# Kernel optimization log

Hardware: AMD Instinct MI355X
Metric: run time of the kernel (lower is better)

## Reference

```python
import jax, jax.numpy as jnp
import numpy as np

PI2 = 6.283185307


def setup_inputs() -> dict:
    key = jax.random.key(0)
    k1, k2, k3, k4 = jax.random.split(key, 4)
    T, n_mix, n_dim = 262144, 64, 16
    data = jax.random.normal(k1, (T, n_dim), dtype=jnp.float32)
    # mixture weights: positive, roughly summing to 1
    wghts = jax.random.uniform(k2, (n_mix, 1), dtype=jnp.float32, minval=0.5, maxval=1.5) / n_mix
    means = jax.random.normal(k3, (n_mix, n_dim), dtype=jnp.float32)
    # diagonal covariances: strictly positive
    dcovs = jax.random.uniform(k4, (n_mix, n_dim), dtype=jnp.float32, minval=0.5, maxval=1.5)
    return {"data": data, "wghts": wghts, "means": means, "dcovs": dcovs}


def reference(data, wghts, means, dcovs):
    # data: (T, D); wghts: (M, 1); means: (M, D); dcovs: (M, D)
    n_dim = data.shape[1]
    c = 1.0 / np.sqrt(PI2 ** n_dim)  # Gaussian normalizer (2*pi)^{-D/2}
    c_dets = 1.0 / jnp.sqrt(jnp.prod(dcovs, axis=1))  # (M,) |Sigma|^{-1/2}
    dprecs = 1.0 / dcovs  # (M, D) diagonal precisions
    diff = data[:, None, :] - means[None, :, :]  # (T, M, D)
    mhbs_dist = jnp.einsum('tmd,md->tm', diff * diff, dprecs)  # (T, M)
    probs = (wghts[:, 0] * c * c_dets)[None, :] * jnp.exp(-0.5 * mhbs_dist)  # (T, M)
    likes = jnp.sum(probs, axis=1)  # (T,)
    log_likes = jnp.mean(jnp.log(likes))
    posteriors = probs / likes[:, None]  # (T, M)
    e_means = posteriors @ means  # (T, D) weighted mean of component means
    return (log_likes, e_means)
```

## Files before the change

kernel.cpp:

```cpp
#include <hip/hip_runtime.h>

#define T_TOTAL 262144
#define NBLOCKS 1024
#define NMIX 64
#define NDIM 16

typedef short bf16x8 __attribute__((ext_vector_type(8)));
typedef unsigned short u16x8 __attribute__((ext_vector_type(8)));
typedef unsigned short u16x4 __attribute__((ext_vector_type(4)));
typedef float f32x4 __attribute__((ext_vector_type(4)));

__device__ __forceinline__ unsigned short f2bf(float f) {
    union { float f; unsigned u; } v; v.f = f;
    unsigned r = v.u + 0x7fff + ((v.u >> 16) & 1);
    return (unsigned short)(r >> 16);
}
__device__ __forceinline__ float bf2f(unsigned short s) {
    union { unsigned u; float f; } v; v.u = ((unsigned)s) << 16;
    return v.f;
}

#define L_WH   0
#define L_WL   5120
#define L_MUT  10240
#define L_A2   12544
#define L_RED  12800
#define L_P    12864

__global__ __launch_bounds__(256, 4) void gmm_main(const float* __restrict__ data,
                                                   const float* __restrict__ wghts,
                                                   const float* __restrict__ means,
                                                   const float* __restrict__ dcovs,
                                                   float* __restrict__ out,
                                                   float* __restrict__ part) {
    __shared__ __align__(16) char lds[22080];
    const int tid  = threadIdx.x;
    const int w    = tid >> 6;
    const int lane = tid & 63;
    const int gi   = lane & 15;
    const int gq   = lane >> 4;
    const size_t tblk = (size_t)blockIdx.x * 256;

    {
        const int m  = tid >> 2;
        const int ql = tid & 3;
        const float LOG2E = 1.4426950408889634f;
        const float LOG2_2PI = 2.6514961294723187f;
        const float4 d4 = *(const float4*)(dcovs + m * 16 + ql * 4);
        const float4 m4 = *(const float4*)(means + m * 16 + ql * 4);
        const float wm = wghts[m];
        float dc[4] = {d4.x, d4.y, d4.z, d4.w};
        float mu[4] = {m4.x, m4.y, m4.z, m4.w};
        u16x4 ghv, glv, hhv, hlv;
        float sumlog = 0.0f, qsum = 0.0f;
        unsigned short* mut = (unsigned short*)(lds + L_MUT);
#pragma unroll
        for (int j = 0; j < 4; ++j) {
            float pr = __builtin_amdgcn_rcpf(dc[j]);
            float g = -0.5f * LOG2E * pr;
            float h = LOG2E * pr * mu[j];
            unsigned short gH = f2bf(g), hH = f2bf(h);
            ghv[j] = gH;  glv[j] = f2bf(g - bf2f(gH));
            hhv[j] = hH;  hlv[j] = f2bf(h - bf2f(hH));
            mut[(ql * 4 + j) * 72 + m] = f2bf(mu[j]);
            sumlog += __builtin_amdgcn_logf(dc[j]);
            qsum   += pr * mu[j] * mu[j];
        }
        char* wrh = lds + L_WH + m * 80;
        char* wrl = lds + L_WL + m * 80;
        *(u16x4*)(wrh + ql * 8)      = ghv;
        *(u16x4*)(wrh + 32 + ql * 8) = hhv;
        *(u16x4*)(wrl + ql * 8)      = glv;
        *(u16x4*)(wrl + 32 + ql * 8) = hlv;
        sumlog += __shfl_xor(sumlog, 1); sumlog += __shfl_xor(sumlog, 2);
        qsum   += __shfl_xor(qsum, 1);   qsum   += __shfl_xor(qsum, 2);
        if (ql == 0) {
            float log2C = __builtin_amdgcn_logf(wm) - 8.0f * LOG2_2PI - 0.5f * sumlog;
            ((float*)(lds + L_A2))[m] = log2C - 0.5f * LOG2E * qsum;
        }
    }
    __syncthreads();

    bf16x8 bh[4], bl[4];
    float a2v[4];
#pragma unroll
    for (int c = 0; c < 4; ++c) {
        bh[c] = *(const bf16x8*)(lds + L_WH + (c * 16 + gi) * 80 + gq * 16);
        bl[c] = *(const bf16x8*)(lds + L_WL + (c * 16 + gi) * 80 + gq * 16);
        a2v[c] = ((const float*)(lds + L_A2))[c * 16 + gi];
    }
    bf16x8 mf0 = *(const bf16x8*)(lds + L_MUT + gi * 144 + gq * 16);
    bf16x8 mf1 = *(const bf16x8*)(lds + L_MUT + gi * 144 + 64 + gq * 16);

    char* pbase = lds + L_P + w * 2304;
    float ll_acc = 0.0f;

    const float* xbase = data + (tblk + (size_t)w * 64 + gi) * 16 + (gq & 1) * 8;
    float4 xa = *(const float4*)(xbase);
    float4 xb = *(const float4*)(xbase + 4);
    const bool sq = (gq < 2);

#pragma unroll
    for (int rt = 0; rt < 4; ++rt) {
        float4 na, nb;
        if (rt < 3) {
            na = *(const float4*)(xbase + (rt + 1) * 256);
            nb = *(const float4*)(xbase + (rt + 1) * 256 + 4);
        }

        float xv[8] = {xa.x, xa.y, xa.z, xa.w, xb.x, xb.y, xb.z, xb.w};
        u16x8 ahv, alv;
#pragma unroll
        for (int j = 0; j < 8; ++j) {
            float q = sq ? xv[j] * xv[j] : xv[j];
            unsigned short qh = f2bf(q);
            ahv[j] = qh;
            alv[j] = f2bf(q - bf2f(qh));
        }
        bf16x8 ah = *(bf16x8*)&ahv;
        bf16x8 al = *(bf16x8*)&alv;

        f32x4 pacc[4];
#pragma unroll
        for (int c = 0; c < 4; ++c) {
            f32x4 a = {0.0f, 0.0f, 0.0f, 0.0f};
            a = __builtin_amdgcn_mfma_f32_16x16x32_bf16(al, bh[c], a, 0, 0, 0);
            a = __builtin_amdgcn_mfma_f32_16x16x32_bf16(ah, bl[c], a, 0, 0, 0);
            a = __builtin_amdgcn_mfma_f32_16x16x32_bf16(ah, bh[c], a, 0, 0, 0);
            pacc[c] = a;
        }

        float p[4][4], prow[4], inv[4];
#pragma unroll
        for (int reg = 0; reg < 4; ++reg) {
#pragma unroll
            for (int c = 0; c < 4; ++c)
                p[c][reg] = __builtin_amdgcn_exp2f(pacc[c][reg] + a2v[c]);
            prow[reg] = (p[0][reg] + p[1][reg]) + (p[2][reg] + p[3][reg]);
        }
#pragma unroll
        for (int reg = 0; reg < 4; ++reg) {
            float v = prow[reg];
            v += __shfl_xor(v, 1);  v += __shfl_xor(v, 2);
            v += __shfl_xor(v, 4);  v += __shfl_xor(v, 8);
            v = fmaxf(v, 1e-35f);
            ll_acc += __builtin_amdgcn_logf(v);
            inv[reg] = __builtin_amdgcn_rcpf(v);
        }

#pragma unroll
        for (int c = 0; c < 4; ++c)
#pragma unroll
            for (int reg = 0; reg < 4; ++reg)
                *(unsigned short*)(pbase + (gq * 4 + reg) * 144 + (c * 16 + gi) * 2) =
                    f2bf(p[c][reg]);

        bf16x8 ap0 = *(const bf16x8*)(pbase + gi * 144 + gq * 16);
        bf16x8 ap1 = *(const bf16x8*)(pbase + gi * 144 + 64 + gq * 16);
        f32x4 e = {0.0f, 0.0f, 0.0f, 0.0f};
        e = __builtin_amdgcn_mfma_f32_16x16x32_bf16(ap0, mf0, e, 0, 0, 0);
        e = __builtin_amdgcn_mfma_f32_16x16x32_bf16(ap1, mf1, e, 0, 0, 0);

        size_t trow = tblk + (size_t)w * 64 + rt * 16 + gq * 4;
#pragma unroll
        for (int reg = 0; reg < 4; ++reg)
            out[1 + (trow + reg) * 16 + gi] = e[reg] * inv[reg];

        if (rt < 3) { xa = na; xb = nb; }
    }

    ll_acc += __shfl_xor(ll_acc, 16);
    ll_acc += __shfl_xor(ll_acc, 32);
    if (lane == 0) ((float*)(lds + L_RED))[w] = ll_acc;
    __syncthreads();
    if (tid == 0) {
        float* r = (float*)(lds + L_RED);
        part[blockIdx.x] = (r[0] + r[1]) + (r[2] + r[3]);
    }
}

__global__ void gmm_fin(const float* __restrict__ part, float* __restrict__ out) {
    __shared__ double red[4];
    const int tid = threadIdx.x;
    double s = 0.0;
#pragma unroll
    for (int k = 0; k < 4; ++k) s += (double)part[tid + k * 256];
#pragma unroll
    for (int off = 32; off > 0; off >>= 1) s += __shfl_down(s, off, 64);
    const int wv = tid >> 6, lane = tid & 63;
    if (lane == 0) red[wv] = s;
    __syncthreads();
    if (tid == 0) {
        const double LN2 = 0.6931471805599453;
        double tot = (red[0] + red[1]) + (red[2] + red[3]);
        out[0] = (float)(tot * LN2 / (double)T_TOTAL);
    }
}

extern "C" void kernel_launch(void* const* d_in, const int* in_sizes, int n_in,
                              void* d_out, int out_size, void* d_ws, size_t ws_size,
                              hipStream_t stream) {
    const float* data  = (const float*)d_in[0];
    const float* wghts = (const float*)d_in[1];
    const float* means = (const float*)d_in[2];
    const float* dcovs = (const float*)d_in[3];
    float* out  = (float*)d_out;
    float* part = (float*)d_ws;

    gmm_main<<<NBLOCKS, 256, 0, stream>>>(data, wghts, means, dcovs, out, part);
    gmm_fin<<<1, 256, 0, stream>>>(part, out);
}
```

Measured before the change: 82.79 us.

## Fuse final reduction via last-block atomic and micro-optimize bf16 packing

Drops the separate finalize kernel: each block publishes its partial log-likelihood to a global array, and the last block to arrive (found with an atomic counter) does the double-precision reduction and resets the counter. Float-to-bf16 splitting now uses the packed v_cvt_pk_bf16_f32 instruction, the per-component bias is folded into the MFMA accumulator initialisation, and the row-sum shuffles become DPP adds. This removes one kernel launch and some VALU work. The cost is a global counter that carries state between calls, plus reliance on inline asm and DPP control encodings.

Result: slower. 142.5 us (+72.1%).

```diff
diff --git a/kernel.cpp b/kernel.cpp
--- a/kernel.cpp
+++ b/kernel.cpp
@@ -9,6 +9,7 @@
 typedef unsigned short u16x8 __attribute__((ext_vector_type(8)));
 typedef unsigned short u16x4 __attribute__((ext_vector_type(4)));
 typedef float f32x4 __attribute__((ext_vector_type(4)));
+typedef unsigned u32x4 __attribute__((ext_vector_type(4)));
 
 __device__ __forceinline__ unsigned short f2bf(float f) {
     union { float f; unsigned u; } v; v.f = f;
@@ -19,21 +20,42 @@
     union { unsigned u; float f; } v; v.u = ((unsigned)s) << 16;
     return v.f;
 }
+__device__ __forceinline__ unsigned cvt_pk(float lo, float hi) {
+    unsigned r;
+    asm("v_cvt_pk_bf16_f32 %0, %1, %2" : "=v"(r) : "v"(lo), "v"(hi));
+    return r;
+}
+__device__ __forceinline__ float f_lo(unsigned w) {
+    union { unsigned u; float f; } v; v.u = w << 16; return v.f;
+}
+__device__ __forceinline__ float f_hi(unsigned w) {
+    union { unsigned u; float f; } v; v.u = w & 0xFFFF0000u; return v.f;
+}
+template<int CTRL>
+__device__ __forceinline__ float dpp_add(float v) {
+    union { float f; int i; } s, t;
+    s.f = v;
+    t.i = __builtin_amdgcn_update_dpp(0, s.i, CTRL, 0xf, 0xf, true);
+    return v + t.f;
+}
+
+__device__ float    g_part[NBLOCKS];
+__device__ unsigned g_count;
 
 #define L_WH   0
 #define L_WL   5120
 #define L_MUT  10240
 #define L_A2   12544
 #define L_RED  12800
-#define L_P    12864
+#define L_DRED 12864
+#define L_P    12896
 
 __global__ __launch_bounds__(256, 4) void gmm_main(const float* __restrict__ data,
                                                    const float* __restrict__ wghts,
                                                    const float* __restrict__ means,
                                                    const float* __restrict__ dcovs,
-                                                   float* __restrict__ out,
-                                                   float* __restrict__ part) {
-    __shared__ __align__(16) char lds[22080];
+                                                   float* __restrict__ out) {
+    __shared__ __align__(16) char lds[22112];
     const int tid  = threadIdx.x;
     const int w    = tid >> 6;
     const int lane = tid & 63;
@@ -109,21 +131,24 @@
         }
 
         float xv[8] = {xa.x, xa.y, xa.z, xa.w, xb.x, xb.y, xb.z, xb.w};
-        u16x8 ahv, alv;
-#pragma unroll
-        for (int j = 0; j < 8; ++j) {
-            float q = sq ? xv[j] * xv[j] : xv[j];
-            unsigned short qh = f2bf(q);
-            ahv[j] = qh;
-            alv[j] = f2bf(q - bf2f(qh));
-        }
-        bf16x8 ah = *(bf16x8*)&ahv;
-        bf16x8 al = *(bf16x8*)&alv;
+        u32x4 ahw, alw;
+#pragma unroll
+        for (int jp = 0; jp < 4; ++jp) {
+            float q0 = sq ? xv[2 * jp] * xv[2 * jp]         : xv[2 * jp];
+            float q1 = sq ? xv[2 * jp + 1] * xv[2 * jp + 1] : xv[2 * jp + 1];
+            unsigned h = cvt_pk(q0, q1);
+            ahw[jp] = h;
+            alw[jp] = cvt_pk(q0 - f_lo(h), q1 - f_hi(h));
+        }
+        union { u32x4 wv; bf16x8 hv; } pa, pl;
+        pa.wv = ahw;  pl.wv = alw;
+        bf16x8 ah = pa.hv;
+        bf16x8 al = pl.hv;
 
         f32x4 pacc[4];
 #pragma unroll
         for (int c = 0; c < 4; ++c) {
-            f32x4 a = {0.0f, 0.0f, 0.0f, 0.0f};
+            f32x4 a = {a2v[c], a2v[c], a2v[c], a2v[c]};
             a = __builtin_amdgcn_mfma_f32_16x16x32_bf16(al, bh[c], a, 0, 0, 0);
             a = __builtin_amdgcn_mfma_f32_16x16x32_bf16(ah, bl[c], a, 0, 0, 0);
             a = __builtin_amdgcn_mfma_f32_16x16x32_bf16(ah, bh[c], a, 0, 0, 0);
@@ -135,25 +160,32 @@
         for (int reg = 0; reg < 4; ++reg) {
 #pragma unroll
             for (int c = 0; c < 4; ++c)
-                p[c][reg] = __builtin_amdgcn_exp2f(pacc[c][reg] + a2v[c]);
+                p[c][reg] = __builtin_amdgcn_exp2f(pacc[c][reg]);
             prow[reg] = (p[0][reg] + p[1][reg]) + (p[2][reg] + p[3][reg]);
         }
 #pragma unroll
         for (int reg = 0; reg < 4; ++reg) {
             float v = prow[reg];
-            v += __shfl_xor(v, 1);  v += __shfl_xor(v, 2);
-            v += __shfl_xor(v, 4);  v += __shfl_xor(v, 8);
+            v = dpp_add<0xB1>(v);
+            v = dpp_add<0x4E>(v);
+            v = dpp_add<0x141>(v);
+            v = dpp_add<0x140>(v);
             v = fmaxf(v, 1e-35f);
             ll_acc += __builtin_amdgcn_logf(v);
             inv[reg] = __builtin_amdgcn_rcpf(v);
         }
 
 #pragma unroll
-        for (int c = 0; c < 4; ++c)
-#pragma unroll
-            for (int reg = 0; reg < 4; ++reg)
-                *(unsigned short*)(pbase + (gq * 4 + reg) * 144 + (c * 16 + gi) * 2) =
-                    f2bf(p[c][reg]);
+        for (int c = 0; c < 4; ++c) {
+            unsigned w01 = cvt_pk(p[c][0], p[c][1]);
+            unsigned w23 = cvt_pk(p[c][2], p[c][3]);
+            char* col = pbase + (c * 16 + gi) * 2;
+            *(short*)(col + (gq * 4 + 0) * 144) = (short)(w01 & 0xFFFF);
+            *(short*)(col + (gq * 4 + 1) * 144) = (short)(w01 >> 16);
+            *(short*)(col + (gq * 4 + 2) * 144) = (short)(w23 & 0xFFFF);
+            *(short*)(col + (gq * 4 + 3) * 144) = (short)(w23 >> 16);
+        }
+        asm volatile("" ::: "memory");
 
         bf16x8 ap0 = *(const bf16x8*)(pbase + gi * 144 + gq * 16);
         bf16x8 ap1 = *(const bf16x8*)(pbase + gi * 144 + 64 + gq * 16);
@@ -175,25 +207,30 @@
     __syncthreads();
     if (tid == 0) {
         float* r = (float*)(lds + L_RED);
-        part[blockIdx.x] = (r[0] + r[1]) + (r[2] + r[3]);
-    }
-}
-
-__global__ void gmm_fin(const float* __restrict__ part, float* __restrict__ out) {
-    __shared__ double red[4];
-    const int tid = threadIdx.x;
-    double s = 0.0;
-#pragma unroll
-    for (int k = 0; k < 4; ++k) s += (double)part[tid + k * 256];
-#pragma unroll
-    for (int off = 32; off > 0; off >>= 1) s += __shfl_down(s, off, 64);
-    const int wv = tid >> 6, lane = tid & 63;
-    if (lane == 0) red[wv] = s;
+        float s = (r[0] + r[1]) + (r[2] + r[3]);
+        __hip_atomic_store(&g_part[blockIdx.x], s, __ATOMIC_RELEASE,
+                           __HIP_MEMORY_SCOPE_AGENT);
+        unsigned old = __hip_atomic_fetch_add(&g_count, 1u, __ATOMIC_ACQ_REL,
+                                              __HIP_MEMORY_SCOPE_AGENT);
+        ((unsigned*)(lds + L_RED))[8] = (old == NBLOCKS - 1) ? 1u : 0u;
+    }
     __syncthreads();
-    if (tid == 0) {
-        const double LN2 = 0.6931471805599453;
-        double tot = (red[0] + red[1]) + (red[2] + red[3]);
-        out[0] = (float)(tot * LN2 / (double)T_TOTAL);
+    if (((volatile unsigned*)(lds + L_RED))[8]) {
+        __threadfence();
+        double s = 0.0;
+#pragma unroll
+        for (int k = 0; k < NBLOCKS / 256; ++k) s += (double)g_part[tid + k * 256];
+#pragma unroll
+        for (int off = 32; off > 0; off >>= 1) s += __shfl_down(s, off, 64);
+        if (lane == 0) ((double*)(lds + L_DRED))[w] = s;
+        __syncthreads();
+        if (tid == 0) {
+            const double LN2 = 0.6931471805599453;
+            double* rr = (double*)(lds + L_DRED);
+            double tot = (rr[0] + rr[1]) + (rr[2] + rr[3]);
+            out[0] = (float)(tot * LN2 / (double)T_TOTAL);
+            g_count = 0;
+        }
     }
 }
 
@@ -205,8 +242,7 @@
     const float* means = (const float*)d_in[2];
     const float* dcovs = (const float*)d_in[3];
     float* out  = (float*)d_out;
-    float* part = (float*)d_ws;
-
-    gmm_main<<<NBLOCKS, 256, 0, stream>>>(data, wghts, means, dcovs, out, part);
-    gmm_fin<<<1, 256, 0, stream>>>(part, out);
-}
+    (void)d_ws; (void)ws_size;
+
+    gmm_main<<<NBLOCKS, 256, 0, stream>>>(data, wghts, means, dcovs, out);
+}
```
